# Performance work log

Hardware: AMD Instinct MI355X
Metric: run time of the kernel (lower is better)

Reference implementation:

```python
import jax, jax.numpy as jnp
import numpy as np

B, M, D, K = 64, 2_000_000, 32, 10
EPS = 1e-5            # kernel epsilon in _inverse_kernel
DENOM_C = 1e-5        # denominator_constant in _episodic_reward


def setup_inputs() -> dict:
    key = jax.random.key(0)
    kq, km = jax.random.split(key)
    query = jax.random.normal(kq, (B, D), dtype=jnp.float32)
    memory = jax.random.normal(km, (M, D), dtype=jnp.float32)
    return {"query": query, "memory": memory, "k": K}


def reference(query, memory, k):
    # Squared Euclidean distances [B, M] via the expanded form (no [B,M,D] intermediate).
    q2 = jnp.sum(query * query, axis=-1, keepdims=True)          # [B, 1]
    m2 = jnp.sum(memory * memory, axis=-1)                       # [M]
    sq = jnp.maximum(q2 + m2[None, :] - 2.0 * (query @ memory.T), 0.0)  # [B, M]
    # Running mean of squared distances (vectorized fixed point of RunningMean;
    # stateful numpy update in the original -> no gradient through it).
    mean_sq = jax.lax.stop_gradient(jnp.mean(sq))
    # _inverse_kernel: eps / (d^2 / mean + eps)
    kdist = EPS / (sq / mean_sq + EPS)                           # [B, M]
    # sklearn kneighbors picks the k SMALLEST metric values.
    neg_topk, _ = jax.lax.top_k(-kdist, k)                       # [B, k]
    neighbor_sum = -jnp.sum(neg_topk, axis=-1)                   # [B]
    # episodic reward: 1 / sqrt(sum(neighbor kernel distances) + c)
    return 1.0 / jnp.sqrt(neighbor_sum + DENOM_C)
```

## Files before the change

### kernel.cpp

```cpp
#include <hip/hip_runtime.h>
#include <hip/hip_bf16.h>
#include <float.h>
#include <math.h>

typedef short short8 __attribute__((ext_vector_type(8)));
typedef float f32x4  __attribute__((ext_vector_type(4)));

#define KEPS   1e-5f
#define DENOMC 1e-5f

__device__ __forceinline__ short f2bf(float x) {
    return __builtin_bit_cast(short, __float2bfloat16(x));
}

__device__ __forceinline__ void top10_insert(float (&lst)[10], float s) {
    if (s > lst[0]) {
        lst[0] = s;
        #pragma unroll
        for (int i = 1; i < 10; ++i) {
            float lo = fminf(lst[0], lst[i]);
            float hi = fmaxf(lst[0], lst[i]);
            lst[0] = lo; lst[i] = hi;
        }
    }
}

__global__ __launch_bounds__(256, 5) void ep_main(
    const float* __restrict__ q, const float* __restrict__ mem,
    float* __restrict__ part_top,
    float* __restrict__ part_sums,
    int nb, int ntiles)
{
    const int tid  = threadIdx.x;
    const int lane = tid & 63;
    const int wave = tid >> 6;
    const int g    = lane >> 4;
    const int c    = lane & 15;
    const int bid  = blockIdx.x;

    short8 qfrag[4];
    #pragma unroll
    for (int h = 0; h < 4; ++h) {
        const float* qp = q + (h * 16 + c) * 32 + g * 8;
        float4 w0 = *(const float4*)qp;
        float4 w1 = *(const float4*)(qp + 4);
        short8 f;
        f[0]=f2bf(-2.f*w0.x); f[1]=f2bf(-2.f*w0.y); f[2]=f2bf(-2.f*w0.z); f[3]=f2bf(-2.f*w0.w);
        f[4]=f2bf(-2.f*w1.x); f[5]=f2bf(-2.f*w1.y); f[6]=f2bf(-2.f*w1.z); f[7]=f2bf(-2.f*w1.w);
        qfrag[h] = f;
    }

    float t1[16];
    #pragma unroll
    for (int i = 0; i < 16; ++i) t1[i] = -FLT_MAX;
    float cs[8];
    #pragma unroll
    for (int r = 0; r < 8; ++r) cs[r] = 0.f;
    float sumsq = 0.f;

    const size_t lane_off = (size_t)(wave * 16 + c) * 32 + (size_t)(g * 8);
    const size_t step     = (size_t)nb * 2048;

    auto process = [&](float4 v0, float4 v1) {
        float ps;
        ps = v0.x * v0.x;
        ps = fmaf(v0.y, v0.y, ps);
        ps = fmaf(v0.z, v0.z, ps);
        ps = fmaf(v0.w, v0.w, ps);
        ps = fmaf(v1.x, v1.x, ps);
        ps = fmaf(v1.y, v1.y, ps);
        ps = fmaf(v1.z, v1.z, ps);
        ps = fmaf(v1.w, v1.w, ps);
        sumsq += ps;
        cs[0] += v0.x; cs[1] += v0.y; cs[2] += v0.z; cs[3] += v0.w;
        cs[4] += v1.x; cs[5] += v1.y; cs[6] += v1.z; cs[7] += v1.w;

        float m2 = ps + __shfl_xor(ps, 16, 64);
        m2 = m2 + __shfl_xor(m2, 32, 64);
        f32x4 mi = {m2, m2, m2, m2};

        short8 mf;
        mf[0]=f2bf(v0.x); mf[1]=f2bf(v0.y); mf[2]=f2bf(v0.z); mf[3]=f2bf(v0.w);
        mf[4]=f2bf(v1.x); mf[5]=f2bf(v1.y); mf[6]=f2bf(v1.z); mf[7]=f2bf(v1.w);

        #pragma unroll
        for (int h = 0; h < 4; ++h) {
            f32x4 acc = __builtin_amdgcn_mfma_f32_16x16x32_bf16(qfrag[h], mf, mi, 0, 0, 0);
            t1[h*4+0] = fmaxf(t1[h*4+0], acc[0]);
            t1[h*4+1] = fmaxf(t1[h*4+1], acc[1]);
            t1[h*4+2] = fmaxf(t1[h*4+2], acc[2]);
            t1[h*4+3] = fmaxf(t1[h*4+3], acc[3]);
        }
    };

    const float* p = mem + (size_t)bid * 2048 + lane_off;
    float4 v0 = *(const float4*)p;
    float4 v1 = *(const float4*)(p + 4);
    p += step;
    for (int t = bid + nb; t < ntiles; t += nb) {
        float4 w0 = *(const float4*)p;
        float4 w1 = *(const float4*)(p + 4);
        p += step;
        process(v0, v1);
        v0 = w0; v1 = w1;
    }
    process(v0, v1);

    __shared__ float ltop[64][65];
    __shared__ float red[4][4][8];
    __shared__ float ssred[4];

    const int col = wave * 16 + c;
    #pragma unroll
    for (int h = 0; h < 4; ++h) {
        #pragma unroll
        for (int r = 0; r < 4; ++r)
            ltop[h * 16 + g * 4 + r][col] = t1[h * 4 + r];
    }

    #pragma unroll
    for (int r = 0; r < 8; ++r) {
        float v = cs[r];
        v += __shfl_xor(v, 1, 64);
        v += __shfl_xor(v, 2, 64);
        v += __shfl_xor(v, 4, 64);
        v += __shfl_xor(v, 8, 64);
        cs[r] = v;
    }
    float ssv = sumsq;
    ssv += __shfl_xor(ssv, 1, 64);
    ssv += __shfl_xor(ssv, 2, 64);
    ssv += __shfl_xor(ssv, 4, 64);
    ssv += __shfl_xor(ssv, 8, 64);
    ssv += __shfl_xor(ssv, 16, 64);
    ssv += __shfl_xor(ssv, 32, 64);
    if (c == 0) {
        #pragma unroll
        for (int r = 0; r < 8; ++r) red[wave][g][r] = cs[r];
    }
    if (lane == 0) ssred[wave] = ssv;
    __syncthreads();

    if (tid < 32) {
        float a = red[0][tid >> 3][tid & 7] + red[1][tid >> 3][tid & 7]
                + red[2][tid >> 3][tid & 7] + red[3][tid >> 3][tid & 7];
        part_sums[(size_t)tid * nb + bid] = a;
    } else if (tid == 32) {
        part_sums[(size_t)32 * nb + bid] = ssred[0] + ssred[1] + ssred[2] + ssred[3];
    }

    if (tid < 64) {
        float lst[10];
        #pragma unroll
        for (int i = 0; i < 10; ++i) lst[i] = -FLT_MAX;
        #pragma unroll 4
        for (int s2 = 0; s2 < 64; ++s2) top10_insert(lst, ltop[tid][s2]);
        #pragma unroll
        for (int i = 0; i < 10; ++i)
            part_top[((size_t)tid * nb + bid) * 10 + i] = lst[i];
    }
}

__global__ __launch_bounds__(256) void ep_tail(
    const float* __restrict__ q, const float* __restrict__ part_top,
    const float* __restrict__ part_sums, float* __restrict__ out,
    int nb, int Mrows)
{
    const int b    = blockIdx.x;
    const int tid  = threadIdx.x;
    const int lane = tid & 63;
    const int wave = tid >> 6;

    __shared__ float smem[256 * 33];
    __shared__ float colsum_a[33];
    __shared__ float w4[4];
    __shared__ float mean_s, q2_s;

    if (tid < 64) {
        float x = (tid < 32) ? q[b * 32 + tid] : 0.f;
        float a = x * x;
        a += __shfl_xor(a, 1, 64);
        a += __shfl_xor(a, 2, 64);
        a += __shfl_xor(a, 4, 64);
        a += __shfl_xor(a, 8, 64);
        a += __shfl_xor(a, 16, 64);
        if (tid == 0) q2_s = a;
    }

    float a2 = 0.f;
    #pragma unroll
    for (int e = 0; e < 8; ++e) {
        float x = q[tid * 8 + e];
        a2 = fmaf(x, x, a2);
    }
    a2 += __shfl_xor(a2, 1, 64);
    a2 += __shfl_xor(a2, 2, 64);
    a2 += __shfl_xor(a2, 4, 64);
    a2 += __shfl_xor(a2, 8, 64);
    a2 += __shfl_xor(a2, 16, 64);
    a2 += __shfl_xor(a2, 32, 64);
    if (lane == 0) w4[wave] = a2;

    float acc[33];
    #pragma unroll
    for (int c2 = 0; c2 < 33; ++c2) acc[c2] = 0.f;
    for (int i = tid; i < nb; i += 256) {
        #pragma unroll
        for (int c2 = 0; c2 < 33; ++c2) acc[c2] += part_sums[(size_t)c2 * nb + i];
    }
    #pragma unroll
    for (int c2 = 0; c2 < 33; ++c2) smem[tid * 33 + c2] = acc[c2];
    __syncthreads();
    if (tid < 33) {
        float a = 0.f;
        #pragma unroll 16
        for (int j = 0; j < 256; ++j) a += smem[j * 33 + tid];
        colsum_a[tid] = a;
    }
    __syncthreads();

    if (tid < 32) {
        float qs = 0.f;
        #pragma unroll 8
        for (int bb = 0; bb < 64; ++bb) qs += q[bb * 32 + tid];
        float dq = qs * colsum_a[tid];
        dq += __shfl_xor(dq, 1, 64);
        dq += __shfl_xor(dq, 2, 64);
        dq += __shfl_xor(dq, 4, 64);
        dq += __shfl_xor(dq, 8, 64);
        dq += __shfl_xor(dq, 16, 64);
        if (tid == 0) {
            double q2sum = (double)w4[0] + (double)w4[1] + (double)w4[2] + (double)w4[3];
            double sumsq = (double)colsum_a[32];
            double Md    = (double)Mrows;
            mean_s = (float)((Md * q2sum + 64.0 * sumsq - 2.0 * (double)dq) / (64.0 * Md));
        }
    }
    __syncthreads();

    float lst[10];
    #pragma unroll
    for (int i = 0; i < 10; ++i) lst[i] = -FLT_MAX;
    const float* pt = part_top + (size_t)b * nb * 10;
    for (int i = tid; i < nb; i += 256) {
        const float* pp = pt + (size_t)i * 10;
        #pragma unroll
        for (int r = 0; r < 10; ++r) top10_insert(lst, pp[r]);
    }
    #pragma unroll
    for (int r = 0; r < 10; ++r) smem[tid * 10 + r] = lst[r];
    __syncthreads();

    if (tid < 32) {
        float m[10];
        #pragma unroll
        for (int i = 0; i < 10; ++i) m[i] = -FLT_MAX;
        for (int j2 = 0; j2 < 8; ++j2) {
            #pragma unroll
            for (int r = 0; r < 10; ++r) top10_insert(m, smem[(tid * 8 + j2) * 10 + r]);
        }
        #pragma unroll
        for (int r = 0; r < 10; ++r) smem[2560 + tid * 10 + r] = m[r];
    }
    __syncthreads();

    if (tid == 0) {
        float m[10];
        #pragma unroll
        for (int i = 0; i < 10; ++i) m[i] = -FLT_MAX;
        for (int j2 = 0; j2 < 32; ++j2) {
            #pragma unroll
            for (int r = 0; r < 10; ++r) top10_insert(m, smem[2560 + j2 * 10 + r]);
        }
        const float mean = mean_s;
        const float q2b  = q2_s;
        float sum = 0.f;
        #pragma unroll
        for (int r = 0; r < 10; ++r) {
            float sq = m[r] + q2b;
            sq = fmaxf(sq, 0.f);
            sum += KEPS / (sq / mean + KEPS);
        }
        out[b] = 1.0f / sqrtf(sum + DENOMC);
    }
}

extern "C" void kernel_launch(void* const* d_in, const int* in_sizes, int n_in,
                              void* d_out, int out_size, void* d_ws, size_t ws_size,
                              hipStream_t stream)
{
    const float* q   = (const float*)d_in[0];
    const float* mem = (const float*)d_in[1];
    float* out = (float*)d_out;

    const int Mrows  = in_sizes[1] / 32;
    const int ntiles = Mrows / 64;

    int nb = 1280;
    while (nb > 64 && ((size_t)nb * 673 + 64) * sizeof(float) > ws_size) nb >>= 1;
    if (nb > ntiles) nb = ntiles;

    float* part_top  = (float*)d_ws;
    float* part_sums = part_top + (size_t)64 * nb * 10;

    ep_main<<<dim3(nb), dim3(256), 0, stream>>>(q, mem, part_top, part_sums, nb, ntiles);
    ep_tail<<<dim3(64), dim3(256), 0, stream>>>(q, part_top, part_sums, out, nb, Mrows);
}
```

Baseline: 98.95 us.

## Stream memory tiles through double-buffered LDS via direct global-to-LDS loads

Each memory tile is now loaded straight from global memory into LDS with global_load_lds, replacing the per-lane register prefetch. The two LDS buffers alternate, and read offsets are XOR-swizzled to avoid bank conflicts. The intent is to free VGPRs and let the next tile's loads overlap with the MFMA and reduction work on the current one. In exchange it adds two block-wide barriers per tile and an extra LDS read, and the LDS region is reused for the later top-k staging.

Measured after the change: 97.92 us. Within noise of the previous version (-1.0%).

```diff
diff --git a/kernel.cpp b/kernel.cpp
--- a/kernel.cpp
+++ b/kernel.cpp
@@ -11,6 +11,13 @@
 
 __device__ __forceinline__ short f2bf(float x) {
     return __builtin_bit_cast(short, __float2bfloat16(x));
+}
+
+__device__ __forceinline__ void gload_lds16(const void* g, void* l) {
+    __builtin_amdgcn_global_load_lds(
+        (const __attribute__((address_space(1))) void*)g,
+        (__attribute__((address_space(3))) void*)l,
+        16, 0, 0);
 }
 
 __device__ __forceinline__ void top10_insert(float (&lst)[10], float s) {
@@ -31,6 +38,10 @@
     float* __restrict__ part_sums,
     int nb, int ntiles)
 {
+    __shared__ float smem[4224];
+    __shared__ float red[4][4][8];
+    __shared__ float ssred[4];
+
     const int tid  = threadIdx.x;
     const int lane = tid & 63;
     const int wave = tid >> 6;
@@ -42,11 +53,11 @@
     #pragma unroll
     for (int h = 0; h < 4; ++h) {
         const float* qp = q + (h * 16 + c) * 32 + g * 8;
-        float4 w0 = *(const float4*)qp;
-        float4 w1 = *(const float4*)(qp + 4);
+        f32x4 w0 = *(const f32x4*)qp;
+        f32x4 w1 = *(const f32x4*)(qp + 4);
         short8 f;
-        f[0]=f2bf(-2.f*w0.x); f[1]=f2bf(-2.f*w0.y); f[2]=f2bf(-2.f*w0.z); f[3]=f2bf(-2.f*w0.w);
-        f[4]=f2bf(-2.f*w1.x); f[5]=f2bf(-2.f*w1.y); f[6]=f2bf(-2.f*w1.z); f[7]=f2bf(-2.f*w1.w);
+        f[0]=f2bf(-2.f*w0[0]); f[1]=f2bf(-2.f*w0[1]); f[2]=f2bf(-2.f*w0[2]); f[3]=f2bf(-2.f*w0[3]);
+        f[4]=f2bf(-2.f*w1[0]); f[5]=f2bf(-2.f*w1[1]); f[6]=f2bf(-2.f*w1[2]); f[7]=f2bf(-2.f*w1[3]);
         qfrag[h] = f;
     }
 
@@ -58,30 +69,42 @@
     for (int r = 0; r < 8; ++r) cs[r] = 0.f;
     float sumsq = 0.f;
 
-    const size_t lane_off = (size_t)(wave * 16 + c) * 32 + (size_t)(g * 8);
-    const size_t step     = (size_t)nb * 2048;
-
-    auto process = [&](float4 v0, float4 v1) {
+    const int    swz  = ((tid >> 3) & 3) << 1;
+    const size_t off0 = (size_t)(tid ^ swz) * 16;
+    char* lds_d0[2], * lds_d1[2];
+    #pragma unroll
+    for (int b = 0; b < 2; ++b) {
+        lds_d0[b] = (char*)smem + b * 8192 + wave * 1024;
+        lds_d1[b] = (char*)smem + b * 8192 + 4096 + wave * 1024;
+    }
+    const int    Y0    = wave * 128 + c * 8 + g * 2;
+    const size_t rdoff = (size_t)(Y0 ^ ((c & 3) << 1)) * 16;
+
+    auto process = [&](const float* buf) {
+        const f32x4* rp = (const f32x4*)((const char*)buf + rdoff);
+        f32x4 v0 = rp[0];
+        f32x4 v1 = rp[1];
+
         float ps;
-        ps = v0.x * v0.x;
-        ps = fmaf(v0.y, v0.y, ps);
-        ps = fmaf(v0.z, v0.z, ps);
-        ps = fmaf(v0.w, v0.w, ps);
-        ps = fmaf(v1.x, v1.x, ps);
-        ps = fmaf(v1.y, v1.y, ps);
-        ps = fmaf(v1.z, v1.z, ps);
-        ps = fmaf(v1.w, v1.w, ps);
+        ps = v0[0] * v0[0];
+        ps = fmaf(v0[1], v0[1], ps);
+        ps = fmaf(v0[2], v0[2], ps);
+        ps = fmaf(v0[3], v0[3], ps);
+        ps = fmaf(v1[0], v1[0], ps);
+        ps = fmaf(v1[1], v1[1], ps);
+        ps = fmaf(v1[2], v1[2], ps);
+        ps = fmaf(v1[3], v1[3], ps);
         sumsq += ps;
-        cs[0] += v0.x; cs[1] += v0.y; cs[2] += v0.z; cs[3] += v0.w;
-        cs[4] += v1.x; cs[5] += v1.y; cs[6] += v1.z; cs[7] += v1.w;
+        cs[0] += v0[0]; cs[1] += v0[1]; cs[2] += v0[2]; cs[3] += v0[3];
+        cs[4] += v1[0]; cs[5] += v1[1]; cs[6] += v1[2]; cs[7] += v1[3];
 
         float m2 = ps + __shfl_xor(ps, 16, 64);
         m2 = m2 + __shfl_xor(m2, 32, 64);
         f32x4 mi = {m2, m2, m2, m2};
 
         short8 mf;
-        mf[0]=f2bf(v0.x); mf[1]=f2bf(v0.y); mf[2]=f2bf(v0.z); mf[3]=f2bf(v0.w);
-        mf[4]=f2bf(v1.x); mf[5]=f2bf(v1.y); mf[6]=f2bf(v1.z); mf[7]=f2bf(v1.w);
+        mf[0]=f2bf(v0[0]); mf[1]=f2bf(v0[1]); mf[2]=f2bf(v0[2]); mf[3]=f2bf(v0[3]);
+        mf[4]=f2bf(v1[0]); mf[5]=f2bf(v1[1]); mf[6]=f2bf(v1[2]); mf[7]=f2bf(v1[3]);
 
         #pragma unroll
         for (int h = 0; h < 4; ++h) {
@@ -93,22 +116,30 @@
         }
     };
 
-    const float* p = mem + (size_t)bid * 2048 + lane_off;
-    float4 v0 = *(const float4*)p;
-    float4 v1 = *(const float4*)(p + 4);
-    p += step;
-    for (int t = bid + nb; t < ntiles; t += nb) {
-        float4 w0 = *(const float4*)p;
-        float4 w1 = *(const float4*)(p + 4);
-        p += step;
-        process(v0, v1);
-        v0 = w0; v1 = w1;
-    }
-    process(v0, v1);
-
-    __shared__ float ltop[64][65];
-    __shared__ float red[4][4][8];
-    __shared__ float ssred[4];
+    const char*  msrc = (const char*)mem + (size_t)bid * 8192 + off0;
+    const size_t step = (size_t)nb * 8192;
+
+    gload_lds16(msrc,        lds_d0[0]);
+    gload_lds16(msrc + 4096, lds_d1[0]);
+    msrc += step;
+
+    int t = bid, cur = 0;
+    for (;;) {
+        __syncthreads();
+        const bool more = (t + nb) < ntiles;
+        if (more) {
+            gload_lds16(msrc,        lds_d0[cur ^ 1]);
+            gload_lds16(msrc + 4096, lds_d1[cur ^ 1]);
+            msrc += step;
+        }
+        process(smem + cur * 2048);
+        if (!more) break;
+        __syncthreads();
+        cur ^= 1; t += nb;
+    }
+
+    __syncthreads();
+    float (*ltop)[65] = (float (*)[65])smem;
 
     const int col = wave * 16 + c;
     #pragma unroll
```
